# Kernel tuning notes

Hardware: AMD Instinct MI355X
Metric: run time of the kernel (lower is better)

Reference implementation:

```python
import jax, jax.numpy as jnp
import numpy as np


def _mlp(x, W1, b1, W2, b2):
    # Dropout layers are identity at inference (p=0.2 in train only).
    h = jax.nn.relu(jnp.einsum('bsi,ih->bsh', x, W1) + b1)
    return jax.nn.relu(jnp.einsum('bsh,hk->bsk', h, W2) + b2)


def setup_inputs() -> dict:
    key = jax.random.key(0)
    ks = jax.random.split(key, 4)
    B_, S, D_in, H = 32, 1024, 768, 1024
    A = jax.random.normal(ks[0], (B_, S, D_in), dtype=jnp.float32)
    B = jax.random.normal(ks[1], (B_, S, D_in), dtype=jnp.float32)
    W1 = jax.random.normal(ks[2], (D_in, H), dtype=jnp.float32) * (1.0 / np.sqrt(D_in))
    b1 = jnp.zeros((H,), dtype=jnp.float32)
    W2 = jax.random.normal(ks[3], (H, H), dtype=jnp.float32) * (1.0 / np.sqrt(H))
    b2 = jnp.zeros((H,), dtype=jnp.float32)
    return {"A": A, "B": B, "W1": W1, "b1": b1, "W2": W2, "b2": b2}


def reference(A, B, W1, b1, W2, b2):
    f_A = _mlp(A, W1, b1, W2, b2)           # [b, S, H]
    f_B = _mlp(B, W1, b1, W2, b2)           # [b, S, H]
    e = jnp.einsum('bih,bjh->bij', f_A, f_B)  # [b, S_A, S_B] unscaled scores
    beta = jnp.einsum('bij,bjd->bid', jax.nn.softmax(e, axis=-1), B)
    # alpha = softmax(e^T, -1) @ B  (note: B, exactly as in the source code)
    alpha = jnp.einsum('bji,bjd->bid', jax.nn.softmax(jnp.swapaxes(e, 1, 2), axis=-1), B)
    return (beta, alpha)
```

## Files before the change

kernel.cpp:

```cpp
#include <hip/hip_runtime.h>
#include <hip/hip_bf16.h>

typedef __attribute__((ext_vector_type(8))) short bf16x8;
typedef __attribute__((ext_vector_type(4))) float f32x4;

__device__ __forceinline__ unsigned short f2bf(float f) {
  union { float f; unsigned u; } v; v.f = f;
  unsigned r = v.u + 0x7FFFu + ((v.u >> 16) & 1u);
  return (unsigned short)(r >> 16);
}

__device__ __forceinline__ void gl_lds16(const void* g, void* l) {
  __builtin_amdgcn_global_load_lds(
      (__attribute__((address_space(1))) void*)(g),
      (__attribute__((address_space(3))) void*)(l), 16, 0, 0);
}

__global__ __launch_bounds__(256) void k_convert(const float* __restrict__ in,
                                                 unsigned short* __restrict__ out,
                                                 int n8) {
  int i = blockIdx.x * 256 + threadIdx.x;
  if (i >= n8) return;
  const float4* ip = (const float4*)in;
  float4 v0 = ip[2 * i], v1 = ip[2 * i + 1];
  ushort4 o0 = make_ushort4(f2bf(v0.x), f2bf(v0.y), f2bf(v0.z), f2bf(v0.w));
  ushort4 o1 = make_ushort4(f2bf(v1.x), f2bf(v1.y), f2bf(v1.z), f2bf(v1.w));
  ((ushort4*)out)[2 * i] = o0;
  ((ushort4*)out)[2 * i + 1] = o1;
}

template <typename OutT>
__global__ __launch_bounds__(256) void k_transpose(const float* __restrict__ in,
                                                   OutT* __restrict__ out,
                                                   int R, int C,
                                                   long inStride, long outStride) {
  __shared__ float tile[64][65];
  const float* ib = in + (long)blockIdx.z * inStride;
  OutT* ob = out + (long)blockIdx.z * outStride;
  int tc = blockIdx.x * 64;
  int tr = blockIdx.y * 64;
  int t = threadIdx.x;
  int lr = t >> 4;
  int lc = (t & 15) * 4;
#pragma unroll
  for (int rr = 0; rr < 64; rr += 16) {
    float4 v = *(const float4*)&ib[(long)(tr + rr + lr) * C + tc + lc];
    tile[rr + lr][lc + 0] = v.x;
    tile[rr + lr][lc + 1] = v.y;
    tile[rr + lr][lc + 2] = v.z;
    tile[rr + lr][lc + 3] = v.w;
  }
  __syncthreads();
#pragma unroll
  for (int ii = 0; ii < 64; ii += 16) {
    int i = ii + lr;
    if constexpr (sizeof(OutT) == 2) {
      ushort4 w = make_ushort4(f2bf(tile[lc + 0][i]), f2bf(tile[lc + 1][i]),
                               f2bf(tile[lc + 2][i]), f2bf(tile[lc + 3][i]));
      *(ushort4*)&ob[(long)(tc + i) * R + tr + lc] = w;
    } else {
      float4 w = make_float4(tile[lc + 0][i], tile[lc + 1][i],
                             tile[lc + 2][i], tile[lc + 3][i]);
      *(float4*)&ob[(long)(tc + i) * R + tr + lc] = w;
    }
  }
}

__global__ __launch_bounds__(256) void k_convtrans_B(const float* __restrict__ in,
                                                     unsigned short* __restrict__ xbf,
                                                     unsigned short* __restrict__ bt) {
  __shared__ float tile[64][65];
  const int bz = blockIdx.z;
  const float* ib = in + (long)bz * 786432L;
  unsigned short* ob = bt + (long)bz * 786432L;
  int tc = blockIdx.x * 64;
  int tr = blockIdx.y * 64;
  int t = threadIdx.x;
  int lr = t >> 4;
  int lc = (t & 15) * 4;
#pragma unroll
  for (int rr = 0; rr < 64; rr += 16) {
    float4 v = *(const float4*)&ib[(long)(tr + rr + lr) * 768 + tc + lc];
    tile[rr + lr][lc + 0] = v.x;
    tile[rr + lr][lc + 1] = v.y;
    tile[rr + lr][lc + 2] = v.z;
    tile[rr + lr][lc + 3] = v.w;
    ushort4 w = make_ushort4(f2bf(v.x), f2bf(v.y), f2bf(v.z), f2bf(v.w));
    *(ushort4*)&xbf[(long)(32768 + bz * 1024 + tr + rr + lr) * 768 + tc + lc] = w;
  }
  __syncthreads();
#pragma unroll
  for (int ii = 0; ii < 64; ii += 16) {
    int i = ii + lr;
    ushort4 w = make_ushort4(f2bf(tile[lc + 0][i]), f2bf(tile[lc + 1][i]),
                             f2bf(tile[lc + 2][i]), f2bf(tile[lc + 3][i]));
    *(ushort4*)&ob[(long)(tc + i) * 1024 + tr + lc] = w;
  }
}

__global__ __launch_bounds__(256) void k_colstats(const float* __restrict__ E,
                                                  float* __restrict__ colMp,
                                                  float* __restrict__ colSp) {
  const float* e = E + (long)blockIdx.y * 1048576L + (long)blockIdx.x * 131072L +
                   threadIdx.x * 4;
  float m0 = -3.4e38f, m1 = -3.4e38f, m2 = -3.4e38f, m3 = -3.4e38f;
  float s0 = 0.f, s1 = 0.f, s2 = 0.f, s3 = 0.f;
  for (int r = 0; r < 128; ++r) {
    float4 v = *(const float4*)(e + (long)r * 1024);
    float n0 = fmaxf(m0, v.x); s0 = s0 * __expf(m0 - n0) + __expf(v.x - n0); m0 = n0;
    float n1 = fmaxf(m1, v.y); s1 = s1 * __expf(m1 - n1) + __expf(v.y - n1); m1 = n1;
    float n2 = fmaxf(m2, v.z); s2 = s2 * __expf(m2 - n2) + __expf(v.z - n2); m2 = n2;
    float n3 = fmaxf(m3, v.w); s3 = s3 * __expf(m3 - n3) + __expf(v.w - n3); m3 = n3;
  }
  long o = ((long)blockIdx.y * 8 + blockIdx.x) * 1024 + threadIdx.x * 4;
  *(float4*)&colMp[o] = make_float4(m0, m1, m2, m3);
  *(float4*)&colSp[o] = make_float4(s0, s1, s2, s3);
}

__global__ __launch_bounds__(256) void k_colcombine(const float* __restrict__ colMp,
                                                    const float* __restrict__ colSp,
                                                    float* __restrict__ colM,
                                                    float* __restrict__ colIS) {
  int idx = blockIdx.x * 256 + threadIdx.x;
  int b = idx >> 10, c = idx & 1023;
  float m = -3.4e38f;
  float mc[8], sc[8];
#pragma unroll
  for (int k = 0; k < 8; ++k) {
    mc[k] = colMp[((long)b * 8 + k) * 1024 + c];
    sc[k] = colSp[((long)b * 8 + k) * 1024 + c];
    m = fmaxf(m, mc[k]);
  }
  float s = 0.f;
#pragma unroll
  for (int k = 0; k < 8; ++k) s += sc[k] * __expf(mc[k] - m);
  colM[idx] = m;
  colIS[idx] = 1.0f / s;
}

__global__ __launch_bounds__(256) void k_softmax(const float* __restrict__ E,
                                                 unsigned short* __restrict__ P,
                                                 unsigned short* __restrict__ P2,
                                                 const float* __restrict__ colM,
                                                 const float* __restrict__ colIS) {
  long row = blockIdx.x;
  const float* e = E + row * 1024;
  int t = threadIdx.x;
  float4 v = *(const float4*)&e[t * 4];
  float m = fmaxf(fmaxf(v.x, v.y), fmaxf(v.z, v.w));
#pragma unroll
  for (int o = 32; o; o >>= 1) m = fmaxf(m, __shfl_xor(m, o));
  __shared__ float red[4];
  __shared__ float red2[4];
  int wid = t >> 6;
  if ((t & 63) == 0) red[wid] = m;
  __syncthreads();
  m = fmaxf(fmaxf(red[0], red[1]), fmaxf(red[2], red[3]));
  float p0 = __expf(v.x - m), p1 = __expf(v.y - m);
  float p2 = __expf(v.z - m), p3 = __expf(v.w - m);
  float s = p0 + p1 + p2 + p3;
#pragma unroll
  for (int o = 32; o; o >>= 1) s += __shfl_xor(s, o);
  if ((t & 63) == 0) red2[wid] = s;
  __syncthreads();
  s = red2[0] + red2[1] + red2[2] + red2[3];
  float inv = 1.0f / s;
  *(ushort4*)&P[row * 1024 + t * 4] =
      make_ushort4(f2bf(p0 * inv), f2bf(p1 * inv), f2bf(p2 * inv), f2bf(p3 * inv));
  long cb = (row >> 10) * 1024 + t * 4;
  float4 cm = *(const float4*)&colM[cb];
  float4 ci = *(const float4*)&colIS[cb];
  *(ushort4*)&P2[row * 1024 + t * 4] =
      make_ushort4(f2bf(__expf(v.x - cm.x) * ci.x), f2bf(__expf(v.y - cm.y) * ci.y),
                   f2bf(__expf(v.z - cm.z) * ci.z), f2bf(__expf(v.w - cm.w) * ci.w));
}

template <bool BIAS_RELU, bool OUT_BF16>
__global__ __launch_bounds__(256, 2) void k_gemm_bt(
    const unsigned short* __restrict__ A, long lda, long aBatch,
    const unsigned short* __restrict__ A2,
    const unsigned short* __restrict__ Bt, long ldb, long bBatch,
    void* __restrict__ C, void* __restrict__ C2, long ldc, long cBatch,
    const float* __restrict__ bias, int K, int zsplit) {
  __shared__ unsigned short As[128 * 64];
  __shared__ unsigned short Bs[256 * 64];
  const int t = threadIdx.x;
  const int w = t >> 6, l = t & 63;
  const int lr = l & 15, lh = l >> 4;
  const int wm = w >> 1, wn = w & 1;

  const int gx = gridDim.x, gy = gridDim.y;
  const int nwg = gx * gy * gridDim.z;
  const int hw = blockIdx.x + gx * (blockIdx.y + gy * blockIdx.z);
  const int q = nwg >> 3;
  const int logical = (hw & 7) * q + (hw >> 3);
  const int bx = logical % gx;
  const int rem = logical / gx;
  const int by = rem % gy;
  int bz = rem / gy;

  const unsigned short* Abase = A;
  void* Cbase = C;
  if (bz >= zsplit) { Abase = A2; Cbase = C2; bz -= zsplit; }

  const long m0 = (long)by * 128;
  const long n0 = (long)bx * 256;
  const unsigned short* Ab = Abase + (long)bz * aBatch;
  const unsigned short* Bb = Bt + (long)bz * bBatch;

  const int srow = t >> 3;
  const int sc16 = (t & 7) ^ (srow & 7);
  const int scol = sc16 * 8;
  const unsigned short* ag = Ab + (m0 + srow) * lda + scol;
  const unsigned short* bg = Bb + (n0 + srow) * ldb + scol;
  unsigned short* al = &As[srow * 64 + (t & 7) * 8];
  unsigned short* bl = &Bs[srow * 64 + (t & 7) * 8];

  f32x4 acc[4][8];
#pragma unroll
  for (int i = 0; i < 4; ++i)
#pragma unroll
    for (int j = 0; j < 8; ++j) acc[i][j] = (f32x4){0.f, 0.f, 0.f, 0.f};

  for (int k0 = 0; k0 < K; k0 += 64) {
#pragma unroll
    for (int j = 0; j < 4; ++j)
      gl_lds16(ag + (long)(j * 32) * lda + k0, al + j * 2048);
#pragma unroll
    for (int j = 0; j < 8; ++j)
      gl_lds16(bg + (long)(j * 32) * ldb + k0, bl + j * 2048);
    __syncthreads();
#pragma unroll
    for (int kk = 0; kk < 2; ++kk) {
      const int rsw = ((kk * 4 + lh) ^ (lr & 7)) * 8;
      bf16x8 af[4], bfr[8];
#pragma unroll
      for (int m = 0; m < 4; ++m)
        af[m] = *(const bf16x8*)&As[(wm * 64 + m * 16 + lr) * 64 + rsw];
#pragma unroll
      for (int n = 0; n < 8; ++n)
        bfr[n] = *(const bf16x8*)&Bs[(wn * 128 + n * 16 + lr) * 64 + rsw];
#pragma unroll
      for (int m = 0; m < 4; ++m)
#pragma unroll
        for (int n = 0; n < 8; ++n)
          acc[m][n] = __builtin_amdgcn_mfma_f32_16x16x32_bf16(af[m], bfr[n], acc[m][n], 0, 0, 0);
    }
    __syncthreads();
  }

  const long crow = m0 + wm * 64;
  const long ccol = n0 + wn * 128;
#pragma unroll
  for (int n = 0; n < 8; ++n) {
    const long col = ccol + n * 16 + lr;
    float bv = 0.f;
    if constexpr (BIAS_RELU) bv = bias[col];
#pragma unroll
    for (int m = 0; m < 4; ++m) {
      f32x4 v = acc[m][n];
#pragma unroll
      for (int r = 0; r < 4; ++r) {
        const long rrow = crow + m * 16 + lh * 4 + r;
        float x = v[r];
        if constexpr (BIAS_RELU) x = fmaxf(x + bv, 0.f);
        if constexpr (OUT_BF16)
          ((unsigned short*)Cbase)[(long)bz * cBatch + rrow * ldc + col] = f2bf(x);
        else
          ((float*)Cbase)[(long)bz * cBatch + rrow * ldc + col] = x;
      }
    }
  }
}

extern "C" void kernel_launch(void* const* d_in, const int* in_sizes, int n_in,
                              void* d_out, int out_size, void* d_ws, size_t ws_size,
                              hipStream_t stream) {
  const float* A_in = (const float*)d_in[0];
  const float* B_in = (const float*)d_in[1];
  const float* W1 = (const float*)d_in[2];
  const float* b1 = (const float*)d_in[3];
  const float* W2 = (const float*)d_in[4];
  const float* b2 = (const float*)d_in[5];

  char* ws = (char*)d_ws;
  unsigned short* Xbf  = (unsigned short*)(ws + 0L);
  unsigned short* H    = (unsigned short*)(ws + 100663296L);
  unsigned short* F    = (unsigned short*)(ws + 234881024L);
  unsigned short* BinT = (unsigned short*)(ws + 369098752L);
  unsigned short* W1T  = (unsigned short*)(ws + 419430400L);
  unsigned short* W2T  = (unsigned short*)(ws + 421003264L);
  unsigned short* P    = (unsigned short*)(ws + 0L);
  unsigned short* P2   = (unsigned short*)(ws + 234881024L);
  float* colMp = (float*)(ws + 100663296L);
  float* colSp = (float*)(ws + 100663296L + 1048576L);
  float* colM  = (float*)(ws + 100663296L + 2097152L);
  float* colIS = (float*)(ws + 100663296L + 2228224L);
  float* E  = (float*)d_out;
  float* beta = (float*)d_out;
  float* alpha = (float*)d_out + 25165824L;
  const int NOSPLIT = 1 << 30;

  k_convert<<<12288, 256, 0, stream>>>(A_in, Xbf, 3145728);
  k_convtrans_B<<<dim3(12, 16, 32), 256, 0, stream>>>(B_in, Xbf, BinT);
  k_transpose<unsigned short><<<dim3(16, 12, 1), 256, 0, stream>>>(W1, W1T, 768, 1024, 0, 0);
  k_transpose<unsigned short><<<dim3(16, 16, 1), 256, 0, stream>>>(W2, W2T, 1024, 1024, 0, 0);

  k_gemm_bt<true, true><<<dim3(4, 512, 1), 256, 0, stream>>>(
      Xbf, 768, 0, nullptr, W1T, 768, 0, (void*)H, nullptr, 1024, 0, b1, 768, NOSPLIT);
  k_gemm_bt<true, true><<<dim3(4, 512, 1), 256, 0, stream>>>(
      H, 1024, 0, nullptr, W2T, 1024, 0, (void*)F, nullptr, 1024, 0, b2, 1024, NOSPLIT);

  k_gemm_bt<false, false><<<dim3(4, 8, 32), 256, 0, stream>>>(
      F, 1024, 1048576L, nullptr, F + 33554432L, 1024, 1048576L, (void*)E, nullptr,
      1024, 1048576L, nullptr, 1024, NOSPLIT);

  k_colstats<<<dim3(8, 32), 256, 0, stream>>>(E, colMp, colSp);
  k_colcombine<<<128, 256, 0, stream>>>(colMp, colSp, colM, colIS);
  k_softmax<<<32768, 256, 0, stream>>>(E, P, P2, colM, colIS);

  k_gemm_bt<false, false><<<dim3(3, 8, 64), 256, 0, stream>>>(
      P, 1024, 1048576L, P2, BinT, 1024, 786432L, (void*)beta, (void*)alpha,
      768, 786432L, nullptr, 1024, 32);
}
```

Before: 670.3 us.

## Fuse row and column softmax statistics into the score GEMM epilogue

The score GEMM epilogue now computes per-tile row and column max and sum-of-exp from the accumulators and writes partial stats. A single combine kernel merges them, and the softmax kernel no longer does block reductions. This removes a full extra read of the 128MB E matrix by the column-stats kernel and drops the in-kernel reductions. In exchange the GEMM epilogue gains shuffle and exp work plus an LDS barrier.

```diff
diff --git a/kernel.cpp b/kernel.cpp
--- a/kernel.cpp
+++ b/kernel.cpp
@@ -98,75 +98,60 @@
   }
 }
 
-__global__ __launch_bounds__(256) void k_colstats(const float* __restrict__ E,
-                                                  float* __restrict__ colMp,
-                                                  float* __restrict__ colSp) {
-  const float* e = E + (long)blockIdx.y * 1048576L + (long)blockIdx.x * 131072L +
-                   threadIdx.x * 4;
-  float m0 = -3.4e38f, m1 = -3.4e38f, m2 = -3.4e38f, m3 = -3.4e38f;
-  float s0 = 0.f, s1 = 0.f, s2 = 0.f, s3 = 0.f;
-  for (int r = 0; r < 128; ++r) {
-    float4 v = *(const float4*)(e + (long)r * 1024);
-    float n0 = fmaxf(m0, v.x); s0 = s0 * __expf(m0 - n0) + __expf(v.x - n0); m0 = n0;
-    float n1 = fmaxf(m1, v.y); s1 = s1 * __expf(m1 - n1) + __expf(v.y - n1); m1 = n1;
-    float n2 = fmaxf(m2, v.z); s2 = s2 * __expf(m2 - n2) + __expf(v.z - n2); m2 = n2;
-    float n3 = fmaxf(m3, v.w); s3 = s3 * __expf(m3 - n3) + __expf(v.w - n3); m3 = n3;
-  }
-  long o = ((long)blockIdx.y * 8 + blockIdx.x) * 1024 + threadIdx.x * 4;
-  *(float4*)&colMp[o] = make_float4(m0, m1, m2, m3);
-  *(float4*)&colSp[o] = make_float4(s0, s1, s2, s3);
-}
-
-__global__ __launch_bounds__(256) void k_colcombine(const float* __restrict__ colMp,
-                                                    const float* __restrict__ colSp,
-                                                    float* __restrict__ colM,
-                                                    float* __restrict__ colIS) {
+__global__ __launch_bounds__(256) void k_statcombine(
+    const float* __restrict__ rowPM, const float* __restrict__ rowPS,
+    const float* __restrict__ colPM, const float* __restrict__ colPS,
+    float* __restrict__ rowM, float* __restrict__ rowIS,
+    float* __restrict__ colM, float* __restrict__ colIS) {
   int idx = blockIdx.x * 256 + threadIdx.x;
-  int b = idx >> 10, c = idx & 1023;
-  float m = -3.4e38f;
-  float mc[8], sc[8];
-#pragma unroll
-  for (int k = 0; k < 8; ++k) {
-    mc[k] = colMp[((long)b * 8 + k) * 1024 + c];
-    sc[k] = colSp[((long)b * 8 + k) * 1024 + c];
-    m = fmaxf(m, mc[k]);
-  }
-  float s = 0.f;
-#pragma unroll
-  for (int k = 0; k < 8; ++k) s += sc[k] * __expf(mc[k] - m);
-  colM[idx] = m;
-  colIS[idx] = 1.0f / s;
+  if (idx < 32768) {
+    int z = idx >> 10, i = idx & 1023;
+    float mv[4], sv[4];
+    float m = -3.4e38f;
+#pragma unroll
+    for (int k = 0; k < 4; ++k) {
+      mv[k] = rowPM[((long)z * 4 + k) * 1024 + i];
+      sv[k] = rowPS[((long)z * 4 + k) * 1024 + i];
+      m = fmaxf(m, mv[k]);
+    }
+    float s = 0.f;
+#pragma unroll
+    for (int k = 0; k < 4; ++k) s += sv[k] * __expf(mv[k] - m);
+    rowM[idx] = m;
+    rowIS[idx] = 1.0f / s;
+  } else {
+    int j = idx - 32768;
+    int z = j >> 10, c = j & 1023;
+    float mv[8], sv[8];
+    float m = -3.4e38f;
+#pragma unroll
+    for (int k = 0; k < 8; ++k) {
+      mv[k] = colPM[((long)z * 8 + k) * 1024 + c];
+      sv[k] = colPS[((long)z * 8 + k) * 1024 + c];
+      m = fmaxf(m, mv[k]);
+    }
+    float s = 0.f;
+#pragma unroll
+    for (int k = 0; k < 8; ++k) s += sv[k] * __expf(mv[k] - m);
+    colM[j] = m;
+    colIS[j] = 1.0f / s;
+  }
 }
 
 __global__ __launch_bounds__(256) void k_softmax(const float* __restrict__ E,
                                                  unsigned short* __restrict__ P,
                                                  unsigned short* __restrict__ P2,
+                                                 const float* __restrict__ rowM,
+                                                 const float* __restrict__ rowIS,
                                                  const float* __restrict__ colM,
                                                  const float* __restrict__ colIS) {
   long row = blockIdx.x;
-  const float* e = E + row * 1024;
   int t = threadIdx.x;
-  float4 v = *(const float4*)&e[t * 4];
-  float m = fmaxf(fmaxf(v.x, v.y), fmaxf(v.z, v.w));
-#pragma unroll
-  for (int o = 32; o; o >>= 1) m = fmaxf(m, __shfl_xor(m, o));
-  __shared__ float red[4];
-  __shared__ float red2[4];
-  int wid = t >> 6;
-  if ((t & 63) == 0) red[wid] = m;
-  __syncthreads();
-  m = fmaxf(fmaxf(red[0], red[1]), fmaxf(red[2], red[3]));
-  float p0 = __expf(v.x - m), p1 = __expf(v.y - m);
-  float p2 = __expf(v.z - m), p3 = __expf(v.w - m);
-  float s = p0 + p1 + p2 + p3;
-#pragma unroll
-  for (int o = 32; o; o >>= 1) s += __shfl_xor(s, o);
-  if ((t & 63) == 0) red2[wid] = s;
-  __syncthreads();
-  s = red2[0] + red2[1] + red2[2] + red2[3];
-  float inv = 1.0f / s;
+  float4 v = *(const float4*)&E[row * 1024 + t * 4];
+  float rm = rowM[row], ri = rowIS[row];
   *(ushort4*)&P[row * 1024 + t * 4] =
-      make_ushort4(f2bf(p0 * inv), f2bf(p1 * inv), f2bf(p2 * inv), f2bf(p3 * inv));
+      make_ushort4(f2bf(__expf(v.x - rm) * ri), f2bf(__expf(v.y - rm) * ri),
+                   f2bf(__expf(v.z - rm) * ri), f2bf(__expf(v.w - rm) * ri));
   long cb = (row >> 10) * 1024 + t * 4;
   float4 cm = *(const float4*)&colM[cb];
   float4 ci = *(const float4*)&colIS[cb];
@@ -175,13 +160,15 @@
                    f2bf(__expf(v.z - cm.z) * ci.z), f2bf(__expf(v.w - cm.w) * ci.w));
 }
 
-template <bool BIAS_RELU, bool OUT_BF16>
+template <bool BIAS_RELU, bool OUT_BF16, bool STATS>
 __global__ __launch_bounds__(256, 2) void k_gemm_bt(
     const unsigned short* __restrict__ A, long lda, long aBatch,
     const unsigned short* __restrict__ A2,
     const unsigned short* __restrict__ Bt, long ldb, long bBatch,
     void* __restrict__ C, void* __restrict__ C2, long ldc, long cBatch,
-    const float* __restrict__ bias, int K, int zsplit) {
+    const float* __restrict__ bias, int K, int zsplit,
+    float* __restrict__ rowPM, float* __restrict__ rowPS,
+    float* __restrict__ colPM, float* __restrict__ colPS) {
   __shared__ unsigned short As[128 * 64];
   __shared__ unsigned short Bs[256 * 64];
   const int t = threadIdx.x;
@@ -271,6 +258,75 @@
       }
     }
   }
+
+  if constexpr (STATS) {
+    float* ldsRM = (float*)As;
+    float* ldsRS = (float*)As + 256;
+    float* ldsCM = (float*)Bs;
+    float* ldsCS = (float*)Bs + 512;
+#pragma unroll
+    for (int m = 0; m < 4; ++m) {
+#pragma unroll
+      for (int r = 0; r < 4; ++r) {
+        float lm = acc[m][0][r];
+#pragma unroll
+        for (int n = 1; n < 8; ++n) lm = fmaxf(lm, acc[m][n][r]);
+#pragma unroll
+        for (int o = 1; o < 16; o <<= 1) lm = fmaxf(lm, __shfl_xor(lm, o));
+        float ls = 0.f;
+#pragma unroll
+        for (int n = 0; n < 8; ++n) ls += __expf(acc[m][n][r] - lm);
+#pragma unroll
+        for (int o = 1; o < 16; o <<= 1) ls += __shfl_xor(ls, o);
+        if (lr == 0) {
+          int row = wm * 64 + m * 16 + lh * 4 + r;
+          ldsRM[row * 2 + wn] = lm;
+          ldsRS[row * 2 + wn] = ls;
+        }
+      }
+    }
+#pragma unroll
+    for (int n = 0; n < 8; ++n) {
+      float lm = acc[0][n][0];
+#pragma unroll
+      for (int m = 0; m < 4; ++m)
+#pragma unroll
+        for (int r = 0; r < 4; ++r) lm = fmaxf(lm, acc[m][n][r]);
+#pragma unroll
+      for (int o = 16; o < 64; o <<= 1) lm = fmaxf(lm, __shfl_xor(lm, o));
+      float ls = 0.f;
+#pragma unroll
+      for (int m = 0; m < 4; ++m)
+#pragma unroll
+        for (int r = 0; r < 4; ++r) ls += __expf(acc[m][n][r] - lm);
+#pragma unroll
+      for (int o = 16; o < 64; o <<= 1) ls += __shfl_xor(ls, o);
+      if (lh == 0) {
+        int col = wn * 128 + n * 16 + lr;
+        ldsCM[col * 2 + wm] = lm;
+        ldsCS[col * 2 + wm] = ls;
+      }
+    }
+    __syncthreads();
+    if (t < 128) {
+      float m0v = ldsRM[t * 2], m1v = ldsRM[t * 2 + 1];
+      float s0v = ldsRS[t * 2], s1v = ldsRS[t * 2 + 1];
+      float mm = fmaxf(m0v, m1v);
+      float ss = s0v * __expf(m0v - mm) + s1v * __expf(m1v - mm);
+      long o = ((long)bz * 4 + bx) * 1024 + by * 128 + t;
+      rowPM[o] = mm;
+      rowPS[o] = ss;
+    }
+    {
+      float m0v = ldsCM[t * 2], m1v = ldsCM[t * 2 + 1];
+      float s0v = ldsCS[t * 2], s1v = ldsCS[t * 2 + 1];
+      float mm = fmaxf(m0v, m1v);
+      float ss = s0v * __expf(m0v - mm) + s1v * __expf(m1v - mm);
+      long o = ((long)bz * 8 + by) * 1024 + bx * 256 + t;
+      colPM[o] = mm;
+      colPS[o] = ss;
+    }
+  }
 }
 
 extern "C" void kernel_launch(void* const* d_in, const int* in_sizes, int n_in,
@@ -292,10 +348,14 @@
   unsigned short* W2T  = (unsigned short*)(ws + 421003264L);
   unsigned short* P    = (unsigned short*)(ws + 0L);
   unsigned short* P2   = (unsigned short*)(ws + 234881024L);
-  float* colMp = (float*)(ws + 100663296L);
-  float* colSp = (float*)(ws + 100663296L + 1048576L);
-  float* colM  = (float*)(ws + 100663296L + 2097152L);
-  float* colIS = (float*)(ws + 100663296L + 2228224L);
+  float* rowPM = (float*)(ws + 100663296L);
+  float* rowPS = (float*)(ws + 100663296L + 524288L);
+  float* colPM = (float*)(ws + 100663296L + 1048576L);
+  float* colPS = (float*)(ws + 100663296L + 2097152L);
+  float* rowM  = (float*)(ws + 100663296L + 3145728L);
+  float* rowIS = (float*)(ws + 100663296L + 3276800L);
+  float* colM  = (float*)(ws + 100663296L + 3407872L);
+  float* colIS = (float*)(ws + 100663296L + 3538944L);
   float* E  = (float*)d_out;
   float* beta = (float*)d_out;
   float* alpha = (float*)d_out + 25165824L;
@@ -306,20 +366,22 @@
   k_transpose<unsigned short><<<dim3(16, 12, 1), 256, 0, stream>>>(W1, W1T, 768, 1024, 0, 0);
   k_transpose<unsigned short><<<dim3(16, 16, 1), 256, 0, stream>>>(W2, W2T, 1024, 1024, 0, 0);
 
-  k_gemm_bt<true, true><<<dim3(4, 512, 1), 256, 0, stream>>>(
-      Xbf, 768, 0, nullptr, W1T, 768, 0, (void*)H, nullptr, 1024, 0, b1, 768, NOSPLIT);
-  k_gemm_bt<true, true><<<dim3(4, 512, 1), 256, 0, stream>>>(
-      H, 1024, 0, nullptr, W2T, 1024, 0, (void*)F, nullptr, 1024, 0, b2, 1024, NOSPLIT);
-
-  k_gemm_bt<false, false><<<dim3(4, 8, 32), 256, 0, stream>>>(
+  k_gemm_bt<true, true, false><<<dim3(4, 512, 1), 256, 0, stream>>>(
+      Xbf, 768, 0, nullptr, W1T, 768, 0, (void*)H, nullptr, 1024, 0, b1, 768, NOSPLIT,
+      nullptr, nullptr, nullptr, nullptr);
+  k_gemm_bt<true, true, false><<<dim3(4, 512, 1), 256, 0, stream>>>(
+      H, 1024, 0, nullptr, W2T, 1024, 0, (void*)F, nullptr, 1024, 0, b2, 1024, NOSPLIT,
+      nullptr, nullptr, nullptr, nullptr);
+
+  k_gemm_bt<false, false, true><<<dim3(4, 8, 32), 256, 0, stream>>>(
       F, 1024, 1048576L, nullptr, F + 33554432L, 1024, 1048576L, (void*)E, nullptr,
-      1024, 1048576L, nullptr, 1024, NOSPLIT);
-
-  k_colstats<<<dim3(8, 32), 256, 0, stream>>>(E, colMp, colSp);
-  k_colcombine<<<128, 256, 0, stream>>>(colMp, colSp, colM, colIS);
-  k_softmax<<<32768, 256, 0, stream>>>(E, P, P2, colM, colIS);
-
-  k_gemm_bt<false, false><<<dim3(3, 8, 64), 256, 0, stream>>>(
+      1024, 1048576L, nullptr, 1024, NOSPLIT, rowPM, rowPS, colPM, colPS);
+
+  k_statcombine<<<256, 256, 0, stream>>>(rowPM, rowPS, colPM, colPS,
+                                         rowM, rowIS, colM, colIS);
+  k_softmax<<<32768, 256, 0, stream>>>(E, P, P2, rowM, rowIS, colM, colIS);
+
+  k_gemm_bt<false, false, false><<<dim3(3, 8, 64), 256, 0, stream>>>(
       P, 1024, 1048576L, P2, BinT, 1024, 786432L, (void*)beta, (void*)alpha,
-      768, 786432L, nullptr, 1024, 32);
-}
+      768, 786432L, nullptr, 1024, 32, nullptr, nullptr, nullptr, nullptr);
+}
```

Measured after the change: 644.0 us, median of 2. -3.9%, faster.
